# Optimization experiments

Measured on AMD Instinct MI355X. Metric: run time of the kernel, lower is better.

Reference implementation:

```python
import jax, jax.numpy as jnp
import numpy as np

N = 256
IL_MMI = 0.02      # insertion loss MMI
IMB = 0.01         # imbalance MMI
IL_CR = 0.02       # insertion loss Crossing
CT = 0.01          # cross talk Crossing


def _mmi_matrix():
    # 2x2 MMI: sqrt(1-IL)*[[t, i r],[i r, t]] with t=sqrt((1+imb)/2), r=sqrt((1-imb)/2)
    a = np.sqrt(1.0 - IL_MMI)
    t = np.sqrt((1.0 + IMB) / 2.0)
    r = np.sqrt((1.0 - IMB) / 2.0)
    mmi2 = a * np.array([[t, 1j * r], [1j * r, t]], dtype=np.complex64)
    # block-diagonal over even pairs (0,1),(2,3),...
    return jnp.asarray(np.kron(np.eye(N // 2, dtype=np.complex64), mmi2))


def _crossing_matrix():
    # pairs start at odd index 1; rows 0 and N-1 pass through with amplitude sqrt(1-IL)*sqrt(1-CT)
    a = np.sqrt(1.0 - IL_CR)
    thru = a * np.sqrt(1.0 - CT)
    cr2 = a * np.array([[np.sqrt(CT), 1j * np.sqrt(1.0 - CT)],
                        [1j * np.sqrt(1.0 - CT), np.sqrt(CT)]], dtype=np.complex64)
    M = np.zeros((N, N), dtype=np.complex64)
    M[0, 0] = thru
    for i in range(1, N - 1, 2):
        M[i:i + 2, i:i + 2] = cr2
    if N % 2 == 0:
        M[-1, -1] = thru
    return jnp.asarray(M)


def setup_inputs() -> dict:
    key = jax.random.key(0)
    thetas = jax.random.uniform(key, (N // 2 + 2, N), dtype=jnp.float32) * (2.0 * np.pi)
    return {"thetas": thetas}


def reference(thetas):
    MMI = _mmi_matrix()
    CR = _crossing_matrix()
    phases = jnp.exp(1j * thetas)  # [N//2+2, N] complex64; diag phase-shift layers

    # arch = ht[0] @ I  (diagonal left-multiply == row scaling)
    arch0 = jnp.diag(phases[0])

    def body(arch, ph):
        # one mesh stage with trailing crossing (iterations i = 0 .. N//2-2)
        arch = MMI @ arch
        arch = ph[:, None] * arch      # ht[i+1] @ arch
        arch = MMI @ arch
        arch = CR @ arch
        return arch, None

    arch, _ = jax.lax.scan(body, arch0, phases[1:N // 2])

    # last loop iteration (i = N//2-1): no crossing
    arch = MMI @ arch
    arch = phases[N // 2][:, None] * arch
    arch = MMI @ arch
    # final phase layer ht[N//2+1]
    arch = phases[N // 2 + 1][:, None] * arch
    return arch
```

## Files before the change

kernel.cpp:

```cpp
#include <hip/hip_runtime.h>


__device__ __forceinline__ float dpp_up1(float x) {
    return __int_as_float(__builtin_amdgcn_update_dpp(
        __float_as_int(x), __float_as_int(x), 0x138, 0xf, 0xf, false));
}
__device__ __forceinline__ float dpp_dn1(float x) {
    return __int_as_float(__builtin_amdgcn_update_dpp(
        __float_as_int(x), __float_as_int(x), 0x130, 0xf, 0xf, false));
}

__device__ __forceinline__ void sincos4(float4 th, float sn[4], float cs[4]) {
    __sincosf(th.x, &sn[0], &cs[0]);
    __sincosf(th.y, &sn[1], &cs[1]);
    __sincosf(th.z, &sn[2], &cs[2]);
    __sincosf(th.w, &sn[3], &cs[3]);
}

__global__ __launch_bounds__(64)
void coef_kernel(const float* __restrict__ thetas,
                 float* __restrict__ coefs)
{
    const int s0   = blockIdx.x;
    const int lane = threadIdx.x;

    const float U  = 0.98f * 0.505f;
    const float W  = 0.98f * 0.495f;
    const float Gc = 0.98f * sqrtf(0.505f * 0.495f);

    float4 th = *(const float4*)(thetas + (s0 + 1) * 256 + 4 * lane);
    float s[4], c[4];
    sincos4(th, s, c);

    float4 A, B, C;
    A.x = U * c[0] - W * c[1];   A.y = U * s[0] - W * s[1];
    A.z = U * c[1] - W * c[0];   A.w = U * s[1] - W * s[0];
    B.x = -Gc * (s[0] + s[1]);   B.y = Gc * (c[0] + c[1]);
    B.z = -Gc * (s[2] + s[3]);   B.w = Gc * (c[2] + c[3]);
    C.x = U * c[2] - W * c[3];   C.y = U * s[2] - W * s[3];
    C.z = U * c[3] - W * c[2];   C.w = U * s[3] - W * s[2];

    float4* cp = (float4*)coefs;
    cp[0 * 8192 + s0 * 64 + lane] = A;
    cp[1 * 8192 + s0 * 64 + lane] = B;
    cp[2 * 8192 + s0 * 64 + lane] = C;
}

__global__ __launch_bounds__(64, 1)
void neuropuls_mesh_kernel(const float* __restrict__ thetas,
                           const float* __restrict__ coefs,
                           float* __restrict__ out)
{
    constexpr int N = 256;
    const int lane = threadIdx.x;
    const int col  = blockIdx.x;

    const float BT = sqrtf(0.98f * 0.01f);
    const float BR = sqrtf(0.98f * 0.99f);

    float vr[4] = {0.f, 0.f, 0.f, 0.f};
    float vi[4] = {0.f, 0.f, 0.f, 0.f};

    {
        const float th0 = thetas[col];
        float s0, c0;
        __sincosf(th0, &s0, &c0);
        const int r0 = col - 4 * lane;
        if (0 <= r0 && r0 < 4) { vr[r0] = c0; vi[r0] = s0; }
    }

    auto mstep = [&](const float4 A, const float4 B, const float4 C) {
        {
            const float xr = vr[0], xi = vi[0], yr = vr[1], yi = vi[1];
            vr[0] = A.x * xr - A.y * xi + B.x * yr - B.y * yi;
            vi[0] = A.x * xi + A.y * xr + B.x * yi + B.y * yr;
            vr[1] = B.x * xr - B.y * xi + A.z * yr - A.w * yi;
            vi[1] = B.x * xi + B.y * xr + A.z * yi + A.w * yr;
        }
        {
            const float xr = vr[2], xi = vi[2], yr = vr[3], yi = vi[3];
            vr[2] = C.x * xr - C.y * xi + B.z * yr - B.w * yi;
            vi[2] = C.x * xi + C.y * xr + B.z * yi + B.w * yr;
            vr[3] = B.z * xr - B.w * xi + C.z * yr - C.w * yi;
            vi[3] = B.z * xi + B.w * xr + C.z * yi + C.w * yr;
        }
    };

    auto crossing = [&]() {
        float pv3r = dpp_up1(vr[3]);
        float pv3i = dpp_up1(vi[3]);
        float nv0r = dpp_dn1(vr[0]);
        float nv0i = dpp_dn1(vi[0]);
        {
            float xr = vr[1], xi = vi[1], yr = vr[2], yi = vi[2];
            vr[1] = BT * xr - BR * yi;  vi[1] = BT * xi + BR * yr;
            vr[2] = BT * yr - BR * xi;  vi[2] = BT * yi + BR * xr;
        }
        {
            float yr = vr[0], yi = vi[0];
            float nr = BT * yr - BR * pv3i;
            float ni = BT * yi + BR * pv3r;
            vr[0] = (lane == 0) ? BR * yr : nr;
            vi[0] = (lane == 0) ? BR * yi : ni;
        }
        {
            float xr = vr[3], xi = vi[3];
            float nr = BT * xr - BR * nv0i;
            float ni = BT * xi + BR * nv0r;
            vr[3] = (lane == 63) ? BR * xr : nr;
            vi[3] = (lane == 63) ? BR * xi : ni;
        }
    };

    const float4* pA = (const float4*)coefs + lane;
    const float4* pB = (const float4*)coefs + 8192 + lane;
    const float4* pC = (const float4*)coefs + 16384 + lane;

    float4 A0 = pA[0],   B0 = pB[0],   C0 = pC[0];
    float4 A1 = pA[64],  B1 = pB[64],  C1 = pC[64];
    float4 A2 = pA[128], B2 = pB[128], C2 = pC[128];
    pA += 192; pB += 192; pC += 192;

    #pragma unroll 3
    for (int s = 1; s <= 126; ++s) {
        float4 A3 = pA[0], B3 = pB[0], C3 = pC[0];
        pA += 64; pB += 64; pC += 64;
        mstep(A0, B0, C0);
        crossing();
        A0 = A1; B0 = B1; C0 = C1;
        A1 = A2; B1 = B2; C1 = C2;
        A2 = A3; B2 = B3; C2 = C3;
    }

    mstep(A0, B0, C0);
    crossing();

    mstep(A1, B1, C1);

    {
        float4 thF = *(const float4*)(thetas + 129 * N + 4 * lane);
        float sn[4], cs[4];
        sincos4(thF, sn, cs);
        #pragma unroll
        for (int j = 0; j < 4; ++j) {
            float r = vr[j], i = vi[j];
            vr[j] = cs[j] * r - sn[j] * i;
            vi[j] = cs[j] * i + sn[j] * r;
        }
    }

    #pragma unroll
    for (int j = 0; j < 4; ++j) {
        const int idx = (4 * lane + j) * N + col;
        out[idx]         = vr[j];
        out[N * N + idx] = vi[j];
    }
}

extern "C" void kernel_launch(void* const* d_in, const int* in_sizes, int n_in,
                              void* d_out, int out_size, void* d_ws, size_t ws_size,
                              hipStream_t stream)
{
    const float* thetas = (const float*)d_in[0];
    float* out   = (float*)d_out;
    float* coefs = (float*)d_ws;
    (void)in_sizes; (void)n_in; (void)out_size; (void)ws_size;

    coef_kernel<<<dim3(128), dim3(64), 0, stream>>>(thetas, coefs);
    neuropuls_mesh_kernel<<<dim3(256), dim3(64), 0, stream>>>(thetas, coefs, out);
}
```

Before: 82.57 us.

## Stream per-stage coefficients into a double-buffered LDS ring via global_load_lds

The coefficient layout becomes interleaved per stage, so each stage's A, B and C vectors sit next to each other. The mesh kernel no longer keeps a three-stage register prefetch of global loads. Instead it fetches chunks of 8 stages straight into a two-slot LDS buffer with asynchronous global-to-LDS loads, waiting on vmcnt and lgkmcnt, and reads the next stage from LDS one step ahead. The aim is to hide L2/HBM latency on the serial 128-stage chain with a deeper prefetch. In exchange it adds LDS traffic and hand-placed waitcnt ordering that must stay correct.

```diff
diff --git a/kernel.cpp b/kernel.cpp
--- a/kernel.cpp
+++ b/kernel.cpp
@@ -41,9 +41,9 @@
     C.z = U * c[3] - W * c[2];   C.w = U * s[3] - W * s[2];
 
     float4* cp = (float4*)coefs;
-    cp[0 * 8192 + s0 * 64 + lane] = A;
-    cp[1 * 8192 + s0 * 64 + lane] = B;
-    cp[2 * 8192 + s0 * 64 + lane] = C;
+    cp[(s0 * 3 + 0) * 64 + lane] = A;
+    cp[(s0 * 3 + 1) * 64 + lane] = B;
+    cp[(s0 * 3 + 2) * 64 + lane] = C;
 }
 
 __global__ __launch_bounds__(64, 1)
@@ -52,6 +52,8 @@
                            float* __restrict__ out)
 {
     constexpr int N = 256;
+    __shared__ float4 cbuf[2][1536];
+
     const int lane = threadIdx.x;
     const int col  = blockIdx.x;
 
@@ -112,30 +114,61 @@
         }
     };
 
-    const float4* pA = (const float4*)coefs + lane;
-    const float4* pB = (const float4*)coefs + 8192 + lane;
-    const float4* pC = (const float4*)coefs + 16384 + lane;
-
-    float4 A0 = pA[0],   B0 = pB[0],   C0 = pC[0];
-    float4 A1 = pA[64],  B1 = pB[64],  C1 = pC[64];
-    float4 A2 = pA[128], B2 = pB[128], C2 = pC[128];
-    pA += 192; pB += 192; pC += 192;
-
-    #pragma unroll 3
-    for (int s = 1; s <= 126; ++s) {
-        float4 A3 = pA[0], B3 = pB[0], C3 = pC[0];
-        pA += 64; pB += 64; pC += 64;
-        mstep(A0, B0, C0);
-        crossing();
-        A0 = A1; B0 = B1; C0 = C1;
-        A1 = A2; B1 = B2; C1 = C2;
-        A2 = A3; B2 = B3; C2 = C3;
-    }
-
-    mstep(A0, B0, C0);
-    crossing();
-
-    mstep(A1, B1, C1);
+    auto issue_chunk = [&](int c) {
+        const float4* src = (const float4*)coefs + (c * 24) * 64 + lane;
+        float4* dst = &cbuf[c & 1][0];
+        #pragma unroll
+        for (int j = 0; j < 24; ++j)
+            __builtin_amdgcn_global_load_lds(
+                (const __attribute__((address_space(1))) void*)(src + j * 64),
+                (__attribute__((address_space(3))) void*)(dst + j * 64),
+                16, 0, 0);
+    };
+    auto rdc = [&](int cb, int k, float4& A, float4& B, float4& C) {
+        const float4* p = &cbuf[cb][k * 192 + lane];
+        A = p[0]; B = p[64]; C = p[128];
+    };
+
+    issue_chunk(0);
+    issue_chunk(1);
+    asm volatile("s_waitcnt vmcnt(24)" ::: "memory");
+    __builtin_amdgcn_sched_barrier(0);
+
+    float4 cA, cB, cC;
+    rdc(0, 0, cA, cB, cC);
+
+    for (int c = 0; c < 15; ++c) {
+        const int cb = c & 1;
+        #pragma unroll
+        for (int k = 0; k < 8; ++k) {
+            float4 nA, nB, nC;
+            if (k < 7) rdc(cb, k + 1, nA, nB, nC);
+            mstep(cA, cB, cC);
+            crossing();
+            if (k < 7) { cA = nA; cB = nB; cC = nC; }
+        }
+        asm volatile("s_waitcnt lgkmcnt(0)" ::: "memory");
+        if (c < 14) {
+            issue_chunk(c + 2);
+            asm volatile("s_waitcnt vmcnt(24)" ::: "memory");
+        } else {
+            asm volatile("s_waitcnt vmcnt(0)" ::: "memory");
+        }
+        __builtin_amdgcn_sched_barrier(0);
+        rdc((c + 1) & 1, 0, cA, cB, cC);
+    }
+
+    {
+        #pragma unroll
+        for (int k = 0; k < 7; ++k) {
+            float4 nA, nB, nC;
+            rdc(1, k + 1, nA, nB, nC);
+            mstep(cA, cB, cC);
+            crossing();
+            cA = nA; cB = nB; cC = nC;
+        }
+        mstep(cA, cB, cC);
+    }
 
     {
         float4 thF = *(const float4*)(thetas + 129 * N + 4 * lane);
```

After: 77.67 us. 1.06x faster.
